# Performance work log

Hardware: AMD Instinct MI355X
Metric: run time of the kernel (lower is better)

The kernel has to match this reference:

```python
import jax, jax.numpy as jnp
import numpy as np

B, S, D, H = 2, 2048, 2048, 16
HD = D // H  # 128
L = 10  # adapter_len


def setup_inputs() -> dict:
    key = jax.random.key(0)
    ks = jax.random.split(key, 8)
    x = jax.random.normal(ks[0], (B, S, D), dtype=jnp.float32)
    wq = jax.random.normal(ks[1], (D, D), dtype=jnp.float32) * 0.02
    wk = jax.random.normal(ks[2], (D, D), dtype=jnp.float32) * 0.02
    wv = jax.random.normal(ks[3], (D, D), dtype=jnp.float32) * 0.02
    wo = jax.random.normal(ks[4], (D, D), dtype=jnp.float32) * 0.02
    adapter = jax.random.normal(ks[5], (1, L, D), dtype=jnp.float32)
    gate = jax.random.normal(ks[6], (1, H, 1, 1), dtype=jnp.float32) * 0.1
    # rotary frequencies (LLaMA style, theta=10000)
    inv_freq = 1.0 / (10000.0 ** (jnp.arange(0, HD, 2, dtype=jnp.float32) / HD))
    t = jnp.arange(S, dtype=jnp.float32)
    ang = jnp.outer(t, inv_freq)  # [S, HD//2]
    freqs_cos = jnp.cos(ang)
    freqs_sin = jnp.sin(ang)
    # additive causal mask [1,1,S,S]
    mask = jnp.triu(jnp.full((S, S), -1e9, dtype=jnp.float32), k=1)[None, None]
    return {"x": x, "wq": wq, "wk": wk, "wv": wv, "wo": wo,
            "adapter": adapter, "gate": gate,
            "freqs_cos": freqs_cos, "freqs_sin": freqs_sin, "mask": mask}


def _rope(v, cos, sin):
    # v: [B,S,H,HD]; cos/sin: [S, HD//2]; complex multiply on (even, odd) pairs
    v = v.reshape(*v.shape[:-1], HD // 2, 2)
    v0, v1 = v[..., 0], v[..., 1]
    c = cos[None, :, None, :]
    s = sin[None, :, None, :]
    out = jnp.stack([v0 * c - v1 * s, v0 * s + v1 * c], axis=-1)
    return out.reshape(*out.shape[:-2], HD)


def reference(x, wq, wk, wv, wo, adapter, gate, freqs_cos, freqs_sin, mask):
    scale = 1.0 / np.sqrt(HD)
    xq = (x @ wq).reshape(B, S, H, HD)
    xk = (x @ wk).reshape(B, S, H, HD)
    xv = (x @ wv).reshape(B, S, H, HD)
    xq = _rope(xq, freqs_cos, freqs_sin)
    xk = _rope(xk, freqs_cos, freqs_sin)
    # self-attention with additive causal mask
    scores = jnp.einsum('bqhd,bkhd->bhqk', xq, xk) * scale + mask
    probs = jax.nn.softmax(scores.astype(jnp.float32), axis=-1).astype(xq.dtype)
    out = jnp.einsum('bhqk,bkhd->bqhd', probs, xv)  # [B,S,H,HD]
    # gated adapter cross-attention (no rotary on adapter K/V)
    ak = (adapter[0] @ wk).reshape(L, H, HD)
    av = (adapter[0] @ wv).reshape(L, H, HD)
    a_scores = jnp.einsum('bqhd,khd->bhqk', xq, ak) * scale
    a_probs = gate * jax.nn.softmax(a_scores.astype(jnp.float32), axis=-1).astype(xq.dtype)
    out = out + jnp.einsum('bhqk,khd->bqhd', a_probs, av)
    return out.reshape(B, S, D) @ wo
```

## Files before the change

kernel.cpp:

```cpp
#include <hip/hip_runtime.h>


typedef unsigned short ushort_t;
typedef unsigned int uint32;
typedef __attribute__((ext_vector_type(8))) short bf16x8;
typedef __attribute__((ext_vector_type(4))) float f32x4;

__device__ __forceinline__ void async16(void* lds, const void* g) {
  __builtin_amdgcn_global_load_lds((const __attribute__((address_space(1))) void*)g,
                                   (__attribute__((address_space(3))) void*)lds,
                                   16, 0, 0);
}
__device__ __forceinline__ ushort_t f2bf(float f) {
  uint32 u = __float_as_uint(f);
  u += 0x7FFFu + ((u >> 16) & 1u);
  return (ushort_t)(u >> 16);
}
__device__ __forceinline__ float bf2f(ushort_t b) {
  return __uint_as_float(((uint32)b) << 16);
}
__device__ __forceinline__ float dpp_xor1(float v) {
  return __int_as_float(__builtin_amdgcn_update_dpp(
      0, __float_as_int(v), 0xB1, 0xf, 0xf, true));
}
#define DPP_MAX(t, ctrl) \
  t = fmaxf(t, __int_as_float(__builtin_amdgcn_update_dpp( \
      0, __float_as_int(t), (ctrl), 0xf, 0xf, true)))
#define DPP_ADD(t, ctrl) \
  t += __int_as_float(__builtin_amdgcn_update_dpp( \
      0, __float_as_int(t), (ctrl), 0xf, 0xf, true))
__device__ __forceinline__ float rowmax16(float t) {
  DPP_MAX(t, 0xB1);
  DPP_MAX(t, 0x4E);
  t = fmaxf(t, __int_as_float(__builtin_amdgcn_ds_swizzle(
      __float_as_int(t), 0x101F)));
  DPP_MAX(t, 0x128);
  return t;
}
__device__ __forceinline__ float rowsum16(float t) {
  DPP_ADD(t, 0xB1);
  DPP_ADD(t, 0x4E);
  t += __int_as_float(__builtin_amdgcn_ds_swizzle(__float_as_int(t), 0x101F));
  DPP_ADD(t, 0x128);
  return t;
}

__global__ __launch_bounds__(256) void cast_x_kernel(const float* __restrict__ x,
                                                     ushort_t* __restrict__ Xb) {
  size_t i = ((size_t)blockIdx.x * 256 + threadIdx.x) * 8;
  float4 a = *(const float4*)(x + i);
  float4 b = *(const float4*)(x + i + 4);
  uint4 o;
  o.x = (uint32)f2bf(a.x) | ((uint32)f2bf(a.y) << 16);
  o.y = (uint32)f2bf(a.z) | ((uint32)f2bf(a.w) << 16);
  o.z = (uint32)f2bf(b.x) | ((uint32)f2bf(b.y) << 16);
  o.w = (uint32)f2bf(b.z) | ((uint32)f2bf(b.w) << 16);
  *(uint4*)(Xb + i) = o;
}

__global__ __launch_bounds__(256) void rope_pack_kernel(
    const float* __restrict__ fc, const float* __restrict__ fs,
    float2* __restrict__ fcs) {
  int i = blockIdx.x * 256 + threadIdx.x;
  fcs[i] = make_float2(fc[i], fs[i]);
}

__global__ __launch_bounds__(256) void transpose_w_kernel(
    const float* __restrict__ w0, const float* __restrict__ w1,
    const float* __restrict__ w2, const float* __restrict__ w3,
    ushort_t* __restrict__ outBase) {
  const float* W = (blockIdx.z == 0) ? w0 : (blockIdx.z == 1) ? w1
                 : (blockIdx.z == 2) ? w2 : w3;
  ushort_t* Wt = outBase + (size_t)blockIdx.z * 4194304;
  __shared__ float L[64][65];
  int t = threadIdx.x, tc = t & 63, tr = t >> 6;
  int k0 = blockIdx.x * 64, n0 = blockIdx.y * 64;
  for (int i = 0; i < 16; ++i) {
    int r = i * 4 + tr;
    L[r][tc] = W[(size_t)(k0 + r) * 2048 + n0 + tc];
  }
  __syncthreads();
  int tr8 = t >> 5, tc2 = t & 31;
  for (int i = 0; i < 8; ++i) {
    int r = i * 8 + tr8;
    uint32 pk = (uint32)f2bf(L[2 * tc2][r]) | ((uint32)f2bf(L[2 * tc2 + 1][r]) << 16);
    *(uint32*)(Wt + (size_t)(n0 + r) * 2048 + k0 + 2 * tc2) = pk;
  }
}

__global__ __launch_bounds__(256) void adapter_kv_kernel(
    const float* __restrict__ adapter, const float* __restrict__ wk,
    const float* __restrict__ wv, float* __restrict__ ak, float* __restrict__ av) {
  const float* W = blockIdx.z ? wv : wk;
  float* out = blockIdx.z ? av : ak;
  __shared__ float As[10][128];
  int t = threadIdx.x;
  int k0 = blockIdx.y * 128;
  for (int i = t; i < 1280; i += 256)
    As[i >> 7][i & 127] = adapter[(size_t)(i >> 7) * 2048 + k0 + (i & 127)];
  __syncthreads();
  int n = blockIdx.x * 256 + t;
  float acc[10];
#pragma unroll
  for (int l = 0; l < 10; ++l) acc[l] = 0.f;
  for (int kk = 0; kk < 128; ++kk) {
    float wv_ = W[(size_t)(k0 + kk) * 2048 + n];
#pragma unroll
    for (int l = 0; l < 10; ++l) acc[l] += As[l][kk] * wv_;
  }
#pragma unroll
  for (int l = 0; l < 10; ++l) atomicAdd(&out[l * 2048 + n], acc[l]);
}

__global__ __launch_bounds__(256) void adapter_pack_kernel(
    const float* __restrict__ ak, const float* __restrict__ av,
    ushort_t* __restrict__ akb, ushort_t* __restrict__ avb) {
  int t = blockIdx.x * 256 + threadIdx.x;
  if (t < 32768) {
    int h = t >> 11, l = (t >> 7) & 15, d = t & 127;
    akb[t] = (l < 10) ? f2bf(ak[l * 2048 + h * 128 + d]) : (ushort_t)0;
  }
  int h = t >> 12, d = (t >> 5) & 127, l = t & 31;
  avb[t] = (l < 10) ? f2bf(av[l * 2048 + h * 128 + d]) : (ushort_t)0;
}

__global__ __launch_bounds__(256) void gemm_qkv_kernel(
    const ushort_t* __restrict__ A, const ushort_t* __restrict__ Bt,
    ushort_t* __restrict__ outQ, ushort_t* __restrict__ outK,
    ushort_t* __restrict__ Vt,
    const float2* __restrict__ fcs) {
  __shared__ char lds[32768];
  char* ldsA = lds;
  char* ldsB = lds + 16384;
  const int tid = threadIdx.x;
  const int w = tid >> 6, lane = tid & 63, quad = lane >> 4, l15 = lane & 15;
  const int wm = (w >> 1) * 64, wn = (w & 1) * 64;
  const size_t bm0 = (size_t)blockIdx.y * 128, bn0 = (size_t)blockIdx.x * 128;
  const int K = 2048;

  f32x4 zero4 = {0.f, 0.f, 0.f, 0.f};
  f32x4 acc[4][4];
#pragma unroll
  for (int i = 0; i < 4; ++i)
#pragma unroll
    for (int j = 0; j < 4; ++j) acc[i][j] = zero4;

  const int rS = w * 32;
  const int rowOff = lane >> 3;
  const int cph = lane & 7;

  for (int kt = 0; kt < K; kt += 64) {
#pragma unroll
    for (int i = 0; i < 4; ++i) {
      int r0 = rS + i * 8;
      int row = r0 + rowOff;
      int cl = cph ^ (row & 7);
      async16(ldsA + r0 * 128, A + (bm0 + row) * (size_t)K + kt + cl * 8);
      async16(ldsB + r0 * 128, Bt + (bn0 + row) * (size_t)K + kt + cl * 8);
    }
    __syncthreads();
#pragma unroll
    for (int ks = 0; ks < 2; ++ks) {
      bf16x8 af[4], bfv[4];
      int ch = ks * 4 + quad;
#pragma unroll
      for (int tt = 0; tt < 4; ++tt) {
        int ra = wm + tt * 16 + l15;
        af[tt] = *(const bf16x8*)(ldsA + ra * 128 + ((ch ^ (ra & 7)) * 16));
        int rb = wn + tt * 16 + l15;
        bfv[tt] = *(const bf16x8*)(ldsB + rb * 128 + ((ch ^ (rb & 7)) * 16));
      }
#pragma unroll
      for (int i = 0; i < 4; ++i)
#pragma unroll
        for (int j = 0; j < 4; ++j)
          acc[i][j] = __builtin_amdgcn_mfma_f32_16x16x32_bf16(af[i], bfv[j], acc[i][j], 0, 0, 0);
    }
    __syncthreads();
  }

  const int seg = (int)(bn0 >> 11);
  if (seg < 2) {
    ushort_t* ob = (seg == 0) ? outQ : outK;
#pragma unroll
    for (int i = 0; i < 4; ++i)
#pragma unroll
      for (int r = 0; r < 4; ++r) {
        size_t m = bm0 + wm + i * 16 + quad * 4 + r;
        int s = (int)(m & 2047);
#pragma unroll
        for (int j = 0; j < 4; ++j) {
          size_t ngl = bn0 + wn + j * 16 + l15;
          size_t n = ngl & 2047;
          float v = acc[i][j][r];
          float v2 = dpp_xor1(v);
          int fi = ((int)n & 127) >> 1;
          float2 cs = fcs[s * 64 + fi];
          v = (lane & 1) ? (v2 * cs.y + v * cs.x) : (v * cs.x - v2 * cs.y);
          ob[m * 2048 + n] = f2bf(v);
        }
      }
  } else {
    char* T = lds + w * 8192;
#pragma unroll
    for (int i = 0; i < 4; ++i)
#pragma unroll
      for (int j = 0; j < 4; ++j) {
        int nn = j * 16 + l15;
        int md0 = i * 8 + quad * 2;
        uint32 p01 = (uint32)f2bf(acc[i][j][0]) | ((uint32)f2bf(acc[i][j][1]) << 16);
        uint32 p23 = (uint32)f2bf(acc[i][j][2]) | ((uint32)f2bf(acc[i][j][3]) << 16);
        *(uint32*)(T + nn * 128 + ((md0 ^ (nn & 31)) * 4)) = p01;
        *(uint32*)(T + nn * 128 + (((md0 + 1) ^ (nn & 31)) * 4)) = p23;
      }
    const int bh = (int)((bm0 >> 11) * 16 + ((bn0 & 2047) >> 7));
    const int p = lane & 31;
#pragma unroll
    for (int it = 0; it < 32; ++it) {
      int row = it * 2 + (lane >> 5);
      uint32 dv = *(const uint32*)(T + row * 128 + p * 4);
      int md = p ^ (row & 31);
      size_t d = (size_t)(wn + row);
      size_t s = (bm0 & 2047) + wm + 2 * md;
      *(uint32*)(Vt + ((size_t)bh * 128 + d) * 2048 + s) = dv;
    }
  }
}

__global__ __launch_bounds__(256) void gemm_kernel(
    const ushort_t* __restrict__ A, const ushort_t* __restrict__ Bt,
    float* __restrict__ out, int M, int N, int K) {
  __shared__ char ldsA[16384];
  __shared__ char ldsB[16384];
  const int tid = threadIdx.x;
  const int w = tid >> 6, lane = tid & 63, quad = lane >> 4, l15 = lane & 15;
  const int wm = (w >> 1) * 64, wn = (w & 1) * 64;
  const size_t bm0 = (size_t)blockIdx.y * 128, bn0 = (size_t)blockIdx.x * 128;

  f32x4 zero4 = {0.f, 0.f, 0.f, 0.f};
  f32x4 acc[4][4];
#pragma unroll
  for (int i = 0; i < 4; ++i)
#pragma unroll
    for (int j = 0; j < 4; ++j) acc[i][j] = zero4;

  const int rS = w * 32;
  const int rowOff = lane >> 3;
  const int cph = lane & 7;

  for (int kt = 0; kt < K; kt += 64) {
#pragma unroll
    for (int i = 0; i < 4; ++i) {
      int r0 = rS + i * 8;
      int row = r0 + rowOff;
      int cl = cph ^ (row & 7);
      async16(ldsA + r0 * 128, A + (bm0 + row) * (size_t)K + kt + cl * 8);
      async16(ldsB + r0 * 128, Bt + (bn0 + row) * (size_t)K + kt + cl * 8);
    }
    __syncthreads();
#pragma unroll
    for (int ks = 0; ks < 2; ++ks) {
      bf16x8 af[4], bfv[4];
      int ch = ks * 4 + quad;
#pragma unroll
      for (int tt = 0; tt < 4; ++tt) {
        int ra = wm + tt * 16 + l15;
        af[tt] = *(const bf16x8*)(ldsA + ra * 128 + ((ch ^ (ra & 7)) * 16));
        int rb = wn + tt * 16 + l15;
        bfv[tt] = *(const bf16x8*)(ldsB + rb * 128 + ((ch ^ (rb & 7)) * 16));
      }
#pragma unroll
      for (int i = 0; i < 4; ++i)
#pragma unroll
        for (int j = 0; j < 4; ++j)
          acc[i][j] = __builtin_amdgcn_mfma_f32_16x16x32_bf16(af[i], bfv[j], acc[i][j], 0, 0, 0);
    }
    __syncthreads();
  }
#pragma unroll
  for (int i = 0; i < 4; ++i)
#pragma unroll
    for (int r = 0; r < 4; ++r) {
      size_t m = bm0 + wm + i * 16 + quad * 4 + r;
#pragma unroll
      for (int j = 0; j < 4; ++j) {
        size_t n = bn0 + wn + j * 16 + l15;
        out[m * N + n] = acc[i][j][r];
      }
    }
}

__global__ __launch_bounds__(256) void flash_kernel(
    const ushort_t* __restrict__ Qb, const ushort_t* __restrict__ Kb,
    const ushort_t* __restrict__ Vt, const ushort_t* __restrict__ akb,
    const ushort_t* __restrict__ avb, const float* __restrict__ gate,
    ushort_t* __restrict__ Ob) {
  __shared__ char ldsK[16384];
  __shared__ char ldsV[16384];
  __shared__ char ldsP[16384];
  const int tid = threadIdx.x;
  const int w = tid >> 6, lane = tid & 63, quad = lane >> 4, l15 = lane & 15;
  const int idx = blockIdx.x;
  const int p = idx >> 8, c = idx & 255;
  const int u = c >> 4, vv = c & 15;
  const int qt = p ? (15 - u) : u;
  const int hb = (p << 4) | vv;
  const int h = hb >> 1, b = hb & 1;
  const float scale = 0.08838834764831845f;

  bf16x8 ones;
#pragma unroll
  for (int j = 0; j < 8; ++j) ones[j] = (short)0x3F80;

  bf16x8 qf[2][4];
#pragma unroll
  for (int mt = 0; mt < 2; ++mt) {
    size_t qrow = (size_t)qt * 128 + w * 32 + mt * 16 + l15;
    const ushort_t* base = Qb + ((size_t)b * 2048 + qrow) * 2048 + h * 128 + quad * 8;
#pragma unroll
    for (int ds = 0; ds < 4; ++ds) qf[mt][ds] = *(const bf16x8*)(base + ds * 32);
  }

  f32x4 zero4 = {0.f, 0.f, 0.f, 0.f};
  f32x4 oacc[2][8];
  f32x4 osum[2];
  float mrow[2][4];
#pragma unroll
  for (int mt = 0; mt < 2; ++mt) {
#pragma unroll
    for (int n8 = 0; n8 < 8; ++n8) oacc[mt][n8] = zero4;
    osum[mt] = zero4;
#pragma unroll
    for (int r = 0; r < 4; ++r) mrow[mt][r] = -1e30f;
  }

  const int ktmax = 2 * qt + 1;
  for (int kt = 0; kt <= ktmax; ++kt) {
#pragma unroll
    for (int ii = 0; ii < 4; ++ii) {
      int r0 = w * 16 + ii * 4;
      int row = r0 + (lane >> 4);
      int cl = (lane & 15) ^ (row & 15);
      async16(ldsK + r0 * 256,
              Kb + ((size_t)b * 2048 + kt * 64 + row) * 2048 + h * 128 + cl * 8);
    }
#pragma unroll
    for (int ii = 0; ii < 4; ++ii) {
      int d0 = w * 32 + ii * 8;
      int dr = d0 + (lane >> 3);
      int cl = (lane & 7) ^ (dr & 7);
      async16(ldsV + d0 * 128,
              Vt + ((size_t)(b * 16 + h) * 128 + dr) * 2048 + kt * 64 + cl * 8);
    }
    __syncthreads();

    f32x4 sacc[2][4];
#pragma unroll
    for (int mt = 0; mt < 2; ++mt)
#pragma unroll
      for (int nt = 0; nt < 4; ++nt) sacc[mt][nt] = zero4;
#pragma unroll
    for (int ds = 0; ds < 4; ++ds) {
      bf16x8 kf[4];
      int ch = ds * 4 + quad;
#pragma unroll
      for (int nt = 0; nt < 4; ++nt) {
        int row = nt * 16 + l15;
        kf[nt] = *(const bf16x8*)(ldsK + row * 256 + ((ch ^ (row & 15)) * 16));
      }
#pragma unroll
      for (int mt = 0; mt < 2; ++mt)
#pragma unroll
        for (int nt = 0; nt < 4; ++nt)
          sacc[mt][nt] = __builtin_amdgcn_mfma_f32_16x16x32_bf16(qf[mt][ds], kf[nt], sacc[mt][nt], 0, 0, 0);
    }

    const bool domask = (kt >= 2 * qt);
#pragma unroll
    for (int mt = 0; mt < 2; ++mt) {
      float tmax[4] = {-1e30f, -1e30f, -1e30f, -1e30f};
      const int qbase = qt * 128 + w * 32 + mt * 16 + quad * 4;
#pragma unroll
      for (int nt = 0; nt < 4; ++nt) {
        int kg = kt * 64 + nt * 16 + l15;
#pragma unroll
        for (int r = 0; r < 4; ++r) {
          float s = sacc[mt][nt][r] * scale;
          if (domask && kg > qbase + r) s = -1e30f;
          sacc[mt][nt][r] = s;
          tmax[r] = fmaxf(tmax[r], s);
        }
      }
#pragma unroll
      for (int r = 0; r < 4; ++r) {
        float t = rowmax16(tmax[r]);
        float mnew = fmaxf(mrow[mt][r], t);
        float alpha = __expf(mrow[mt][r] - mnew);
        mrow[mt][r] = mnew;
        osum[mt][r] *= alpha;
#pragma unroll
        for (int n8 = 0; n8 < 8; ++n8) oacc[mt][n8][r] *= alpha;
        tmax[r] = mnew;
      }
#pragma unroll
      for (int nt = 0; nt < 4; ++nt) {
        int col = nt * 16 + l15;
#pragma unroll
        for (int r = 0; r < 4; ++r) {
          float pv = __expf(sacc[mt][nt][r] - tmax[r]);
          int prow = w * 32 + mt * 16 + quad * 4 + r;
          int addr = prow * 128 + (((col >> 3) ^ (prow & 7)) * 16) + (col & 7) * 2;
          *(ushort_t*)(ldsP + addr) = f2bf(pv);
        }
      }
    }

#pragma unroll
    for (int ks = 0; ks < 2; ++ks) {
      int ch = ks * 4 + quad;
      bf16x8 pf[2];
#pragma unroll
      for (int mt = 0; mt < 2; ++mt) {
        int prow = w * 32 + mt * 16 + l15;
        pf[mt] = *(const bf16x8*)(ldsP + prow * 128 + ((ch ^ (prow & 7)) * 16));
      }
#pragma unroll
      for (int mt = 0; mt < 2; ++mt)
        osum[mt] = __builtin_amdgcn_mfma_f32_16x16x32_bf16(pf[mt], ones, osum[mt], 0, 0, 0);
#pragma unroll
      for (int n8 = 0; n8 < 8; ++n8) {
        int dr = n8 * 16 + l15;
        bf16x8 vf = *(const bf16x8*)(ldsV + dr * 128 + ((ch ^ (dr & 7)) * 16));
#pragma unroll
        for (int mt = 0; mt < 2; ++mt)
          oacc[mt][n8] = __builtin_amdgcn_mfma_f32_16x16x32_bf16(pf[mt], vf, oacc[mt][n8], 0, 0, 0);
      }
    }
    __syncthreads();
  }

  const float g = gate[h];
  {
    int row = w * 32 + (lane >> 1);
    int koff = 16 + (lane & 1) * 8;
    *(uint4*)(ldsP + row * 80 + koff * 2) = make_uint4(0, 0, 0, 0);
  }
  f32x4 sa[2] = {zero4, zero4};
#pragma unroll
  for (int ds = 0; ds < 4; ++ds) {
    bf16x8 kfa = *(const bf16x8*)(akb + ((size_t)h * 16 + l15) * 128 + ds * 32 + quad * 8);
#pragma unroll
    for (int mt = 0; mt < 2; ++mt)
      sa[mt] = __builtin_amdgcn_mfma_f32_16x16x32_bf16(qf[mt][ds], kfa, sa[mt], 0, 0, 0);
  }
#pragma unroll
  for (int mt = 0; mt < 2; ++mt) {
#pragma unroll
    for (int r = 0; r < 4; ++r) {
      float s = sa[mt][r] * scale;
      if (l15 >= 10) s = -1e30f;
      float mx = rowmax16(s);
      float e = __expf(s - mx);
      float sum = rowsum16(e);
      float pv = g * e / sum;
      int row = w * 32 + mt * 16 + quad * 4 + r;
      *(ushort_t*)(ldsP + row * 80 + l15 * 2) = f2bf(pv);
    }
  }
  bf16x8 paf[2];
#pragma unroll
  for (int mt = 0; mt < 2; ++mt)
    paf[mt] = *(const bf16x8*)(ldsP + (w * 32 + mt * 16 + l15) * 80 + quad * 16);

#pragma unroll
  for (int mt = 0; mt < 2; ++mt) {
    float rl[4];
#pragma unroll
    for (int r = 0; r < 4; ++r) rl[r] = 1.f / osum[mt][r];
#pragma unroll
    for (int n8 = 0; n8 < 8; ++n8)
#pragma unroll
      for (int r = 0; r < 4; ++r) oacc[mt][n8][r] *= rl[r];
  }
#pragma unroll
  for (int n8 = 0; n8 < 8; ++n8) {
    bf16x8 avf = *(const bf16x8*)(avb + ((size_t)h * 128 + n8 * 16 + l15) * 32 + quad * 8);
#pragma unroll
    for (int mt = 0; mt < 2; ++mt)
      oacc[mt][n8] = __builtin_amdgcn_mfma_f32_16x16x32_bf16(paf[mt], avf, oacc[mt][n8], 0, 0, 0);
  }
#pragma unroll
  for (int mt = 0; mt < 2; ++mt) {
    size_t qb0 = (size_t)qt * 128 + w * 32 + mt * 16 + quad * 4;
#pragma unroll
    for (int n8 = 0; n8 < 8; ++n8) {
      size_t col = (size_t)h * 128 + n8 * 16 + l15;
#pragma unroll
      for (int r = 0; r < 4; ++r)
        Ob[((size_t)b * 2048 + qb0 + r) * 2048 + col] = f2bf(oacc[mt][n8][r]);
    }
  }
}

extern "C" void kernel_launch(void* const* d_in, const int* in_sizes, int n_in,
                              void* d_out, int out_size, void* d_ws, size_t ws_size,
                              hipStream_t stream) {
  (void)in_sizes; (void)n_in; (void)out_size; (void)ws_size;
  const float* x       = (const float*)d_in[0];
  const float* wq      = (const float*)d_in[1];
  const float* wk      = (const float*)d_in[2];
  const float* wv      = (const float*)d_in[3];
  const float* wo      = (const float*)d_in[4];
  const float* adapter = (const float*)d_in[5];
  const float* gate    = (const float*)d_in[6];
  const float* fc      = (const float*)d_in[7];
  const float* fs      = (const float*)d_in[8];

  char* ws = (char*)d_ws;
  ushort_t* Xb   = (ushort_t*)(ws + 0);
  ushort_t* WtQ  = (ushort_t*)(ws + 16777216);
  ushort_t* WtO  = (ushort_t*)(ws + 41943040);
  ushort_t* Qb   = (ushort_t*)(ws + 50331648);
  ushort_t* Kb   = (ushort_t*)(ws + 67108864);
  ushort_t* Vt   = (ushort_t*)(ws + 83886080);
  float*    ak   = (float*)   (ws + 100663296);
  float*    av   = (float*)   (ws + 100745216);
  ushort_t* akb  = (ushort_t*)(ws + 100827136);
  ushort_t* avb  = (ushort_t*)(ws + 100892672);
  float2*   fcs  = (float2*)  (ws + 101023744);
  ushort_t* Ob   = Xb;

  cast_x_kernel<<<4096, 256, 0, stream>>>(x, Xb);
  rope_pack_kernel<<<512, 256, 0, stream>>>(fc, fs, fcs);
  transpose_w_kernel<<<dim3(32, 32, 4), 256, 0, stream>>>(wq, wk, wv, wo, WtQ);
  hipMemsetAsync(ak, 0, 163840, stream);
  adapter_kv_kernel<<<dim3(8, 16, 2), 256, 0, stream>>>(adapter, wk, wv, ak, av);
  adapter_pack_kernel<<<256, 256, 0, stream>>>(ak, av, akb, avb);
  gemm_qkv_kernel<<<dim3(48, 32), 256, 0, stream>>>(Xb, WtQ, Qb, Kb, Vt, fcs);
  flash_kernel<<<512, 256, 0, stream>>>(Qb, Kb, Vt, akb, avb, gate, Ob);
  gemm_kernel<<<dim3(16, 32), 256, 0, stream>>>(Ob, WtO, (float*)d_out, 4096, 2048, 2048);
}
```

Before: 458.9 us.

## Rewrite QKV GEMM as 256x256 double-buffered pipelined kernel with grid swizzle

Replaces the 128x128 QKV projection GEMM with a 512-thread 256x256 tile kernel that double-buffers A/B tiles in 128KB of LDS. It prefetches up to two k-steps ahead with explicit vmcnt waits and barriers, interleaves the async loads with MFMA phases, and raises wave priority around the MFMA blocks. It also remaps the 1D grid to group blocks for L2 reuse. The aim is to hide global load latency and cut redundant operand traffic, at the cost of higher register and LDS use. The fragile manual waitcnt scheme could also cause races.

```diff
diff --git a/kernel.cpp b/kernel.cpp
--- a/kernel.cpp
+++ b/kernel.cpp
@@ -124,73 +124,118 @@
   avb[t] = (l < 10) ? f2bf(av[l * 2048 + h * 128 + d]) : (ushort_t)0;
 }
 
-__global__ __launch_bounds__(256) void gemm_qkv_kernel(
+#define BARX() asm volatile("s_barrier" ::: "memory")
+#define LGKM0() asm volatile("s_waitcnt lgkmcnt(0)" ::: "memory")
+#define VMCNT6() asm volatile("s_waitcnt vmcnt(6)" ::: "memory")
+#define VMCNT0() asm volatile("s_waitcnt vmcnt(0)" ::: "memory")
+
+__global__ __launch_bounds__(512, 2) void gemm_qkv256_kernel(
     const ushort_t* __restrict__ A, const ushort_t* __restrict__ Bt,
     ushort_t* __restrict__ outQ, ushort_t* __restrict__ outK,
-    ushort_t* __restrict__ Vt,
-    const float2* __restrict__ fcs) {
-  __shared__ char lds[32768];
-  char* ldsA = lds;
-  char* ldsB = lds + 16384;
+    ushort_t* __restrict__ Vt, const float2* __restrict__ fcs) {
+  __shared__ char lds[131072];
   const int tid = threadIdx.x;
   const int w = tid >> 6, lane = tid & 63, quad = lane >> 4, l15 = lane & 15;
-  const int wm = (w >> 1) * 64, wn = (w & 1) * 64;
-  const size_t bm0 = (size_t)blockIdx.y * 128, bn0 = (size_t)blockIdx.x * 128;
-  const int K = 2048;
-
-  f32x4 zero4 = {0.f, 0.f, 0.f, 0.f};
-  f32x4 acc[4][4];
-#pragma unroll
-  for (int i = 0; i < 4; ++i)
-#pragma unroll
-    for (int j = 0; j < 4; ++j) acc[i][j] = zero4;
-
-  const int rS = w * 32;
-  const int rowOff = lane >> 3;
-  const int cph = lane & 7;
-
-  for (int kt = 0; kt < K; kt += 64) {
-#pragma unroll
-    for (int i = 0; i < 4; ++i) {
-      int r0 = rS + i * 8;
-      int row = r0 + rowOff;
-      int cl = cph ^ (row & 7);
-      async16(ldsA + r0 * 128, A + (bm0 + row) * (size_t)K + kt + cl * 8);
-      async16(ldsB + r0 * 128, Bt + (bn0 + row) * (size_t)K + kt + cl * 8);
-    }
-    __syncthreads();
-#pragma unroll
-    for (int ks = 0; ks < 2; ++ks) {
-      bf16x8 af[4], bfv[4];
-      int ch = ks * 4 + quad;
-#pragma unroll
-      for (int tt = 0; tt < 4; ++tt) {
-        int ra = wm + tt * 16 + l15;
-        af[tt] = *(const bf16x8*)(ldsA + ra * 128 + ((ch ^ (ra & 7)) * 16));
-        int rb = wn + tt * 16 + l15;
-        bfv[tt] = *(const bf16x8*)(ldsB + rb * 128 + ((ch ^ (rb & 7)) * 16));
-      }
-#pragma unroll
-      for (int i = 0; i < 4; ++i)
-#pragma unroll
-        for (int j = 0; j < 4; ++j)
-          acc[i][j] = __builtin_amdgcn_mfma_f32_16x16x32_bf16(af[i], bfv[j], acc[i][j], 0, 0, 0);
-    }
-    __syncthreads();
+  const int wr = w >> 2, wc = w & 3;
+  const int nt = 32;
+
+  const int wg = (blockIdx.x & 7) * 48 + (blockIdx.x >> 3);
+  const size_t bm0 = (size_t)(wg & 15) * 256;
+  const size_t bn0 = (size_t)(wg >> 4) * 256;
+
+  char* const pA0 = lds;
+  char* const pA1 = lds + 32768;
+  char* const pB0 = lds + 65536;
+  char* const pB1 = lds + 98304;
+
+#define PAT(T) ((((T) & 1) ? pA1 : pA0))
+#define PBT(T) ((((T) & 1) ? pB1 : pB0))
+#define SEG16(OP, LDSB, GROW, T)                                               \
+  do {                                                                         \
+    int rr_ = w * 8 + (lane >> 3);                                             \
+    int cl_ = (lane & 7) ^ (rr_ & 7);                                          \
+    async16((LDSB) + w * 1024,                                                 \
+            (OP) + ((GROW) + (size_t)rr_) * 2048 + (size_t)((T) * 64 + cl_ * 8)); \
+  } while (0)
+#define ST_A01(T)                                                   \
+  do { if ((T) < nt) { SEG16(A, PAT(T), bm0, (T));                  \
+                       SEG16(A, PAT(T) + 16384, bm0 + 128, (T)); } } while (0)
+#define ST_A23(T)                                                   \
+  do { if ((T) < nt) { SEG16(A, PAT(T) + 8192, bm0 + 64, (T));      \
+                       SEG16(A, PAT(T) + 24576, bm0 + 192, (T)); } } while (0)
+#define ST_B01(T)                                                   \
+  do { if ((T) < nt) { SEG16(Bt, PBT(T), bn0, (T));                 \
+                       SEG16(Bt, PBT(T) + 8192, bn0 + 64, (T)); } } while (0)
+#define ST_B23(T)                                                   \
+  do { if ((T) < nt) { SEG16(Bt, PBT(T) + 16384, bn0 + 128, (T));   \
+                       SEG16(Bt, PBT(T) + 24576, bn0 + 192, (T)); } } while (0)
+
+  f32x4 acc[8][4];
+  f32x4 z4 = {0.f, 0.f, 0.f, 0.f};
+#pragma unroll
+  for (int i = 0; i < 8; ++i)
+#pragma unroll
+    for (int j = 0; j < 4; ++j) acc[i][j] = z4;
+
+  ST_A01(0); ST_A23(0); ST_B01(0); ST_B23(0);
+  ST_B01(1); ST_B23(1); ST_A01(1);
+  VMCNT6();
+  BARX();
+
+#define APHASE(PI, STAGE_STMT, TAIL_STMT)                                      \
+  do {                                                                         \
+    bf16x8 af[2][2];                                                           \
+    _Pragma("unroll") for (int ii = 0; ii < 2; ++ii) {                         \
+      int arow = wr * 128 + ((PI) * 2 + ii) * 16 + l15;                        \
+      _Pragma("unroll") for (int ks = 0; ks < 2; ++ks)                         \
+        af[ii][ks] = *(const bf16x8*)(pA + arow * 128 +                        \
+                                      (((ks * 4 + quad) ^ (arow & 7)) * 16));  \
+    }                                                                          \
+    STAGE_STMT;                                                                \
+    BARX();                                                                    \
+    LGKM0();                                                                   \
+    __builtin_amdgcn_s_setprio(1);                                             \
+    _Pragma("unroll") for (int ks = 0; ks < 2; ++ks)                           \
+      _Pragma("unroll") for (int ii = 0; ii < 2; ++ii)                         \
+        _Pragma("unroll") for (int j = 0; j < 4; ++j)                          \
+          acc[(PI) * 2 + ii][j] = __builtin_amdgcn_mfma_f32_16x16x32_bf16(     \
+              af[ii][ks], bf[j][ks], acc[(PI) * 2 + ii][j], 0, 0, 0);          \
+    __builtin_amdgcn_s_setprio(0);                                             \
+    TAIL_STMT;                                                                 \
+    BARX();                                                                    \
+  } while (0)
+
+#pragma unroll 2
+  for (int t = 0; t < nt; ++t) {
+    const char* pA = PAT(t);
+    const char* pB = PBT(t);
+    bf16x8 bf[4][2];
+#pragma unroll
+    for (int j = 0; j < 4; ++j) {
+      int brow = wc * 64 + j * 16 + l15;
+#pragma unroll
+      for (int ks = 0; ks < 2; ++ks)
+        bf[j][ks] = *(const bf16x8*)(pB + brow * 128 +
+                                     (((ks * 4 + quad) ^ (brow & 7)) * 16));
+    }
+    APHASE(0, ST_A23(t + 1), (void)0);
+    APHASE(1, ST_B01(t + 2), (void)0);
+    APHASE(2, ST_B23(t + 2), (void)0);
+    APHASE(3, ST_A01(t + 2), { if (t == nt - 2) VMCNT0(); else VMCNT6(); });
   }
 
   const int seg = (int)(bn0 >> 11);
   if (seg < 2) {
-    ushort_t* ob = (seg == 0) ? outQ : outK;
-#pragma unroll
-    for (int i = 0; i < 4; ++i)
+    ushort_t* ob = seg ? outK : outQ;
+#pragma unroll
+    for (int i = 0; i < 8; ++i)
 #pragma unroll
       for (int r = 0; r < 4; ++r) {
-        size_t m = bm0 + wm + i * 16 + quad * 4 + r;
+        size_t m = bm0 + wr * 128 + i * 16 + quad * 4 + r;
         int s = (int)(m & 2047);
 #pragma unroll
         for (int j = 0; j < 4; ++j) {
-          size_t ngl = bn0 + wn + j * 16 + l15;
+          size_t ngl = bn0 + wc * 64 + j * 16 + l15;
           size_t n = ngl & 2047;
           float v = acc[i][j][r];
           float v2 = dpp_xor1(v);
@@ -201,30 +246,42 @@
         }
       }
   } else {
-    char* T = lds + w * 8192;
-#pragma unroll
-    for (int i = 0; i < 4; ++i)
+    char* T = lds + w * 16384;
+#pragma unroll
+    for (int i = 0; i < 8; ++i)
 #pragma unroll
       for (int j = 0; j < 4; ++j) {
         int nn = j * 16 + l15;
-        int md0 = i * 8 + quad * 2;
+        int q0 = i * 4 + quad;
+        int slot = q0 ^ (nn & 31);
         uint32 p01 = (uint32)f2bf(acc[i][j][0]) | ((uint32)f2bf(acc[i][j][1]) << 16);
         uint32 p23 = (uint32)f2bf(acc[i][j][2]) | ((uint32)f2bf(acc[i][j][3]) << 16);
-        *(uint32*)(T + nn * 128 + ((md0 ^ (nn & 31)) * 4)) = p01;
-        *(uint32*)(T + nn * 128 + (((md0 + 1) ^ (nn & 31)) * 4)) = p23;
-      }
-    const int bh = (int)((bm0 >> 11) * 16 + ((bn0 & 2047) >> 7));
-    const int p = lane & 31;
+        *(uint32*)(T + nn * 256 + slot * 8) = p01;
+        *(uint32*)(T + nn * 256 + slot * 8 + 4) = p23;
+      }
+    const int n2b = (int)(bn0 & 2047) + wc * 64;
+    const int h = n2b >> 7;
+    const size_t d0 = (size_t)(n2b & 127);
+    const int b = (int)(bm0 >> 11);
+    const int s0 = (int)(bm0 & 2047) + wr * 128;
+    const size_t bh = (size_t)b * 16 + h;
 #pragma unroll
     for (int it = 0; it < 32; ++it) {
-      int row = it * 2 + (lane >> 5);
-      uint32 dv = *(const uint32*)(T + row * 128 + p * 4);
-      int md = p ^ (row & 31);
-      size_t d = (size_t)(wn + row);
-      size_t s = (bm0 & 2047) + wm + 2 * md;
-      *(uint32*)(Vt + ((size_t)bh * 128 + d) * 2048 + s) = dv;
-    }
-  }
+      int nn = it * 2 + (lane >> 5);
+      int q = lane & 31;
+      int slot = q ^ (nn & 31);
+      uint2 dv = *(const uint2*)(T + nn * 256 + slot * 8);
+      *(uint2*)(Vt + (bh * 128 + d0 + nn) * 2048 + s0 + 4 * q) = dv;
+    }
+  }
+#undef APHASE
+#undef ST_A01
+#undef ST_A23
+#undef ST_B01
+#undef ST_B23
+#undef SEG16
+#undef PAT
+#undef PBT
 }
 
 __global__ __launch_bounds__(256) void gemm_kernel(
@@ -536,7 +593,7 @@
   hipMemsetAsync(ak, 0, 163840, stream);
   adapter_kv_kernel<<<dim3(8, 16, 2), 256, 0, stream>>>(adapter, wk, wv, ak, av);
   adapter_pack_kernel<<<256, 256, 0, stream>>>(ak, av, akb, avb);
-  gemm_qkv_kernel<<<dim3(48, 32), 256, 0, stream>>>(Xb, WtQ, Qb, Kb, Vt, fcs);
+  gemm_qkv256_kernel<<<dim3(384), 512, 0, stream>>>(Xb, WtQ, Qb, Kb, Vt, fcs);
   flash_kernel<<<512, 256, 0, stream>>>(Qb, Kb, Vt, akb, avb, gate, Ob);
   gemm_kernel<<<dim3(16, 32), 256, 0, stream>>>(Ob, WtO, (float*)d_out, 4096, 2048, 2048);
 }
```

After: 458.6 us. No clear change (-0.1%).

## Rewrite QKV and output GEMMs with double-buffered 128x256 pipelined K-loop

Applied to the files above, without the earlier changes.

Both projection GEMMs move to a shared K-loop with 512-thread blocks and 128x256 output tiles. The loop double-buffers LDS and issues async global-to-LDS loads one or two k-steps ahead, splitting each iteration into phases with explicit barriers, vmcnt waits and raised priority around the MFMA bursts. Block indices are remapped into a grouped order to improve L2 reuse. The intent is to hide global load latency and reduce barrier stalls in the baseline's unpipelined loop. In exchange it uses 96KB of LDS per block, and the hand-placed waitcnt/barrier sequence could hide races if any count is off.

```diff
diff --git a/kernel.cpp b/kernel.cpp
--- a/kernel.cpp
+++ b/kernel.cpp
@@ -124,74 +124,131 @@
   avb[t] = (l < 10) ? f2bf(av[l * 2048 + h * 128 + d]) : (ushort_t)0;
 }
 
-__global__ __launch_bounds__(256) void gemm_qkv_kernel(
+#define QK_BARX() asm volatile("s_barrier" ::: "memory")
+#define QK_LGKM0() asm volatile("s_waitcnt lgkmcnt(0)" ::: "memory")
+
+__device__ __forceinline__ void kloop_128x256(
+    char* lds, const ushort_t* __restrict__ A, const ushort_t* __restrict__ Bt,
+    size_t bm0, size_t bn0, f32x4 (&acc)[4][4]) {
+  const int tid = (int)threadIdx.x;
+  const int w = tid >> 6, lane = tid & 63, quad = lane >> 4, l15 = lane & 15;
+  const int wr = (w >> 2) * 64, wc = (w & 3) * 64;
+  const int nt = 32;
+  char* const pA0 = lds;
+  char* const pA1 = lds + 16384;
+  char* const pB0 = lds + 32768;
+  char* const pB1 = lds + 65536;
+
+#define PAT(T) (((T) & 1) ? pA1 : pA0)
+#define PBT(T) (((T) & 1) ? pB1 : pB0)
+#define SEGL(OP, LDSB, GROW, T)                                                \
+  do {                                                                         \
+    int rr_ = w * 8 + (lane >> 3);                                             \
+    int cl_ = (lane & 7) ^ (rr_ & 7);                                          \
+    async16((LDSB) + w * 1024,                                                 \
+            (OP) + ((GROW) + (size_t)rr_) * 2048 + (size_t)((T) * 64 + cl_ * 8)); \
+  } while (0)
+#define ST_A(T)                                                                \
+  do { if ((T) < nt) { SEGL(A, PAT(T), bm0, (T));                              \
+                       SEGL(A, PAT(T) + 8192, bm0 + 64, (T)); } } while (0)
+#define ST_B0(T)                                                               \
+  do { if ((T) < nt) SEGL(Bt, PBT(T), bn0, (T)); } while (0)
+#define ST_B123(T)                                                             \
+  do { if ((T) < nt) { SEGL(Bt, PBT(T) + 8192,  bn0 + 64,  (T));               \
+                       SEGL(Bt, PBT(T) + 16384, bn0 + 128, (T));               \
+                       SEGL(Bt, PBT(T) + 24576, bn0 + 192, (T)); } } while (0)
+
+  ST_A(0); ST_B0(0); ST_B123(0); ST_B123(1);
+  asm volatile("s_waitcnt vmcnt(3)" ::: "memory");
+  QK_BARX();
+
+#pragma unroll 2
+  for (int t = 0; t < nt; ++t) {
+    const char* pA = PAT(t);
+    const char* pB = PBT(t);
+    bf16x8 bfv[4][2];
+#pragma unroll
+    for (int j = 0; j < 4; ++j) {
+      int brow = wc + j * 16 + l15;
+#pragma unroll
+      for (int ks = 0; ks < 2; ++ks)
+        bfv[j][ks] = *(const bf16x8*)(pB + brow * 128 +
+                                      (((ks * 4 + quad) ^ (brow & 7)) * 16));
+    }
+#pragma unroll
+    for (int ph = 0; ph < 2; ++ph) {
+      bf16x8 af[2][2];
+#pragma unroll
+      for (int ii = 0; ii < 2; ++ii) {
+        int arow = wr + (ph * 2 + ii) * 16 + l15;
+#pragma unroll
+        for (int ks = 0; ks < 2; ++ks)
+          af[ii][ks] = *(const bf16x8*)(pA + arow * 128 +
+                                        (((ks * 4 + quad) ^ (arow & 7)) * 16));
+      }
+      if (ph == 0) { ST_A(t + 1); ST_B0(t + 1); }
+      else         { ST_B123(t + 2); }
+      QK_BARX();
+      QK_LGKM0();
+      __builtin_amdgcn_s_setprio(1);
+#pragma unroll
+      for (int ks = 0; ks < 2; ++ks)
+#pragma unroll
+        for (int ii = 0; ii < 2; ++ii)
+#pragma unroll
+          for (int j = 0; j < 4; ++j)
+            acc[ph * 2 + ii][j] = __builtin_amdgcn_mfma_f32_16x16x32_bf16(
+                af[ii][ks], bfv[j][ks], acc[ph * 2 + ii][j], 0, 0, 0);
+      __builtin_amdgcn_s_setprio(0);
+      if (ph == 1) {
+        if (t == nt - 2) asm volatile("s_waitcnt vmcnt(0)" ::: "memory");
+        else             asm volatile("s_waitcnt vmcnt(3)" ::: "memory");
+      }
+      QK_BARX();
+    }
+  }
+#undef PAT
+#undef PBT
+#undef SEGL
+#undef ST_A
+#undef ST_B0
+#undef ST_B123
+}
+
+__global__ __launch_bounds__(512, 2) void gemm_qkv128_kernel(
     const ushort_t* __restrict__ A, const ushort_t* __restrict__ Bt,
     ushort_t* __restrict__ outQ, ushort_t* __restrict__ outK,
-    ushort_t* __restrict__ Vt,
-    const float2* __restrict__ fcs) {
-  __shared__ char lds[32768];
-  char* ldsA = lds;
-  char* ldsB = lds + 16384;
-  const int tid = threadIdx.x;
+    ushort_t* __restrict__ Vt, const float2* __restrict__ fcs) {
+  __shared__ char lds[98304];
+  const int tid = (int)threadIdx.x;
   const int w = tid >> 6, lane = tid & 63, quad = lane >> 4, l15 = lane & 15;
-  const int wm = (w >> 1) * 64, wn = (w & 1) * 64;
-  const size_t bm0 = (size_t)blockIdx.y * 128, bn0 = (size_t)blockIdx.x * 128;
-  const int K = 2048;
-
-  f32x4 zero4 = {0.f, 0.f, 0.f, 0.f};
+  const int wr = (w >> 2) * 64, wc = (w & 3) * 64;
+
+  const int wg = ((int)blockIdx.x & 7) * 96 + ((int)blockIdx.x >> 3);
+  const size_t bm0 = (size_t)(wg & 31) * 128;
+  const size_t bn0 = (size_t)(wg >> 5) * 256;
+
   f32x4 acc[4][4];
+  f32x4 z4 = {0.f, 0.f, 0.f, 0.f};
 #pragma unroll
   for (int i = 0; i < 4; ++i)
 #pragma unroll
-    for (int j = 0; j < 4; ++j) acc[i][j] = zero4;
-
-  const int rS = w * 32;
-  const int rowOff = lane >> 3;
-  const int cph = lane & 7;
-
-  for (int kt = 0; kt < K; kt += 64) {
-#pragma unroll
-    for (int i = 0; i < 4; ++i) {
-      int r0 = rS + i * 8;
-      int row = r0 + rowOff;
-      int cl = cph ^ (row & 7);
-      async16(ldsA + r0 * 128, A + (bm0 + row) * (size_t)K + kt + cl * 8);
-      async16(ldsB + r0 * 128, Bt + (bn0 + row) * (size_t)K + kt + cl * 8);
-    }
-    __syncthreads();
-#pragma unroll
-    for (int ks = 0; ks < 2; ++ks) {
-      bf16x8 af[4], bfv[4];
-      int ch = ks * 4 + quad;
-#pragma unroll
-      for (int tt = 0; tt < 4; ++tt) {
-        int ra = wm + tt * 16 + l15;
-        af[tt] = *(const bf16x8*)(ldsA + ra * 128 + ((ch ^ (ra & 7)) * 16));
-        int rb = wn + tt * 16 + l15;
-        bfv[tt] = *(const bf16x8*)(ldsB + rb * 128 + ((ch ^ (rb & 7)) * 16));
-      }
-#pragma unroll
-      for (int i = 0; i < 4; ++i)
-#pragma unroll
-        for (int j = 0; j < 4; ++j)
-          acc[i][j] = __builtin_amdgcn_mfma_f32_16x16x32_bf16(af[i], bfv[j], acc[i][j], 0, 0, 0);
-    }
-    __syncthreads();
-  }
+    for (int j = 0; j < 4; ++j) acc[i][j] = z4;
+
+  kloop_128x256(lds, A, Bt, bm0, bn0, acc);
 
   const int seg = (int)(bn0 >> 11);
   if (seg < 2) {
-    ushort_t* ob = (seg == 0) ? outQ : outK;
+    ushort_t* ob = seg ? outK : outQ;
 #pragma unroll
     for (int i = 0; i < 4; ++i)
 #pragma unroll
       for (int r = 0; r < 4; ++r) {
-        size_t m = bm0 + wm + i * 16 + quad * 4 + r;
+        size_t m = bm0 + wr + i * 16 + quad * 4 + r;
         int s = (int)(m & 2047);
 #pragma unroll
         for (int j = 0; j < 4; ++j) {
-          size_t ngl = bn0 + wn + j * 16 + l15;
-          size_t n = ngl & 2047;
+          size_t n = (bn0 + wc + j * 16 + l15) & 2047;
           float v = acc[i][j][r];
           float v2 = dpp_xor1(v);
           int fi = ((int)n & 127) >> 1;
@@ -213,79 +270,52 @@
         *(uint32*)(T + nn * 128 + ((md0 ^ (nn & 31)) * 4)) = p01;
         *(uint32*)(T + nn * 128 + (((md0 + 1) ^ (nn & 31)) * 4)) = p23;
       }
-    const int bh = (int)((bm0 >> 11) * 16 + ((bn0 & 2047) >> 7));
-    const int p = lane & 31;
+    const int b = (int)(bm0 >> 11);
+    const int s0 = (int)(bm0 & 2047) + wr;
+    const int n2 = (int)(bn0 & 2047) + wc;
 #pragma unroll
     for (int it = 0; it < 32; ++it) {
       int row = it * 2 + (lane >> 5);
-      uint32 dv = *(const uint32*)(T + row * 128 + p * 4);
-      int md = p ^ (row & 31);
-      size_t d = (size_t)(wn + row);
-      size_t s = (bm0 & 2047) + wm + 2 * md;
-      *(uint32*)(Vt + ((size_t)bh * 128 + d) * 2048 + s) = dv;
-    }
-  }
-}
-
-__global__ __launch_bounds__(256) void gemm_kernel(
+      int pp = lane & 31;
+      uint32 dv = *(const uint32*)(T + row * 128 + pp * 4);
+      int md = pp ^ (row & 31);
+      int nloc = n2 + row;
+      size_t bh = (size_t)b * 16 + (nloc >> 7);
+      *(uint32*)(Vt + (bh * 128 + (size_t)(nloc & 127)) * 2048 + s0 + 2 * md) = dv;
+    }
+  }
+}
+
+__global__ __launch_bounds__(512, 2) void gemm_wo_kernel(
     const ushort_t* __restrict__ A, const ushort_t* __restrict__ Bt,
-    float* __restrict__ out, int M, int N, int K) {
-  __shared__ char ldsA[16384];
-  __shared__ char ldsB[16384];
-  const int tid = threadIdx.x;
+    float* __restrict__ out) {
+  __shared__ char lds[98304];
+  const int tid = (int)threadIdx.x;
   const int w = tid >> 6, lane = tid & 63, quad = lane >> 4, l15 = lane & 15;
-  const int wm = (w >> 1) * 64, wn = (w & 1) * 64;
-  const size_t bm0 = (size_t)blockIdx.y * 128, bn0 = (size_t)blockIdx.x * 128;
-
-  f32x4 zero4 = {0.f, 0.f, 0.f, 0.f};
+  const int wr = (w >> 2) * 64, wc = (w & 3) * 64;
+
+  const int wg = ((int)blockIdx.x & 7) * 32 + ((int)blockIdx.x >> 3);
+  const size_t bm0 = (size_t)(wg & 31) * 128;
+  const size_t bn0 = (size_t)(wg >> 5) * 256;
+
   f32x4 acc[4][4];
+  f32x4 z4 = {0.f, 0.f, 0.f, 0.f};
 #pragma unroll
   for (int i = 0; i < 4; ++i)
 #pragma unroll
-    for (int j = 0; j < 4; ++j) acc[i][j] = zero4;
-
-  const int rS = w * 32;
-  const int rowOff = lane >> 3;
-  const int cph = lane & 7;
-
-  for (int kt = 0; kt < K; kt += 64) {
-#pragma unroll
-    for (int i = 0; i < 4; ++i) {
-      int r0 = rS + i * 8;
-      int row = r0 + rowOff;
-      int cl = cph ^ (row & 7);
-      async16(ldsA + r0 * 128, A + (bm0 + row) * (size_t)K + kt + cl * 8);
-      async16(ldsB + r0 * 128, Bt + (bn0 + row) * (size_t)K + kt + cl * 8);
-    }
-    __syncthreads();
-#pragma unroll
-    for (int ks = 0; ks < 2; ++ks) {
-      bf16x8 af[4], bfv[4];
-      int ch = ks * 4 + quad;
-#pragma unroll
-      for (int tt = 0; tt < 4; ++tt) {
-        int ra = wm + tt * 16 + l15;
-        af[tt] = *(const bf16x8*)(ldsA + ra * 128 + ((ch ^ (ra & 7)) * 16));
-        int rb = wn + tt * 16 + l15;
-        bfv[tt] = *(const bf16x8*)(ldsB + rb * 128 + ((ch ^ (rb & 7)) * 16));
-      }
-#pragma unroll
-      for (int i = 0; i < 4; ++i)
-#pragma unroll
-        for (int j = 0; j < 4; ++j)
-          acc[i][j] = __builtin_amdgcn_mfma_f32_16x16x32_bf16(af[i], bfv[j], acc[i][j], 0, 0, 0);
-    }
-    __syncthreads();
-  }
+    for (int j = 0; j < 4; ++j) acc[i][j] = z4;
+
+  kloop_128x256(lds, A, Bt, bm0, bn0, acc);
+
 #pragma unroll
   for (int i = 0; i < 4; ++i)
 #pragma unroll
     for (int r = 0; r < 4; ++r) {
-      size_t m = bm0 + wm + i * 16 + quad * 4 + r;
+      size_t m = bm0 + wr + i * 16 + quad * 4 + r;
 #pragma unroll
       for (int j = 0; j < 4; ++j) {
-        size_t n = bn0 + wn + j * 16 + l15;
-        out[m * N + n] = acc[i][j][r];
+        size_t n = bn0 + wc + j * 16 + l15;
+        out[m * 2048 + n] = acc[i][j][r];
       }
     }
 }
@@ -536,7 +566,7 @@
   hipMemsetAsync(ak, 0, 163840, stream);
   adapter_kv_kernel<<<dim3(8, 16, 2), 256, 0, stream>>>(adapter, wk, wv, ak, av);
   adapter_pack_kernel<<<256, 256, 0, stream>>>(ak, av, akb, avb);
-  gemm_qkv_kernel<<<dim3(48, 32), 256, 0, stream>>>(Xb, WtQ, Qb, Kb, Vt, fcs);
+  gemm_qkv128_kernel<<<dim3(768), 512, 0, stream>>>(Xb, WtQ, Qb, Kb, Vt, fcs);
   flash_kernel<<<512, 256, 0, stream>>>(Qb, Kb, Vt, akb, avb, gate, Ob);
-  gemm_kernel<<<dim3(16, 32), 256, 0, stream>>>(Ob, WtO, (float*)d_out, 4096, 2048, 2048);
-}
+  gemm_wo_kernel<<<dim3(256), 512, 0, stream>>>(Ob, WtO, (float*)d_out);
+}
```

Result: faster. 444.9 us (-3.1%).
